# Optimization experiments

Measured on AMD Instinct MI355X. Metric: run time of the kernel, lower is better.

Reference implementation:

```python
import jax, jax.numpy as jnp
import numpy as np

B, T, DE, DD, A, FN, FS = 32, 2000, 512, 1024, 128, 32, 16
TEMPERATURE = 1.0


def setup_inputs() -> dict:
    key = jax.random.key(0)
    ks = jax.random.split(key, 10)
    input_enc = jax.random.normal(ks[0], (B, T, DE), dtype=jnp.float32)
    # lengths in [T//2, T] so no zero-length utterances
    enc_lengths = jax.random.randint(ks[1], (B,), T // 2, T + 1, dtype=jnp.int32)
    input_dec = jax.random.normal(ks[2], (B, DD), dtype=jnp.float32)
    # prev_att: previous-step attention weights (masked, normalized)
    prev_att = jax.random.uniform(ks[3], (B, T), dtype=jnp.float32)
    pad = jnp.arange(T)[None, :] >= enc_lengths[:, None]
    prev_att = jnp.where(pad, 0.0, prev_att)
    prev_att = prev_att / jnp.sum(prev_att, axis=1, keepdims=True)
    # parameters
    conv_w = jax.random.normal(ks[4], (FN, 1, 2 * FS + 1), dtype=jnp.float32) * 0.1  # [out,in,k]
    enc_w = jax.random.normal(ks[5], (A, DE), dtype=jnp.float32) * 0.04
    dec_w = jax.random.normal(ks[6], (A, DD), dtype=jnp.float32) * 0.03
    att_w = jax.random.normal(ks[7], (A, FN), dtype=jnp.float32) * 0.17
    att_b = jnp.zeros((A,), dtype=jnp.float32)
    out_w = jax.random.normal(ks[8], (1, A), dtype=jnp.float32) * 0.09
    return dict(input_enc=input_enc, enc_lengths=enc_lengths, input_dec=input_dec,
                prev_att=prev_att, conv_w=conv_w, enc_w=enc_w, dec_w=dec_w,
                att_w=att_w, att_b=att_b, out_w=out_w)


def reference(input_enc, enc_lengths, input_dec, prev_att,
              conv_w, enc_w, dec_w, att_w, att_b, out_w):
    b, t, _ = input_enc.shape
    fs = (conv_w.shape[-1] - 1) // 2  # 'same' padding
    # padding mask: True at padded positions t >= length
    mask = jnp.arange(t)[None, :] >= enc_lengths[:, None]  # [B,T]
    # location features: Conv1d over prev attention, 1 -> FN channels, same length
    conv = jax.lax.conv_general_dilated(
        prev_att[:, None, :], conv_w, window_strides=(1,),
        padding=[(fs, fs)], dimension_numbers=("NCH", "OIH", "NCH"))  # [B,FN,T]
    loc_feat = conv.transpose(0, 2, 1)  # [B,T,FN]
    projected_att = loc_feat @ att_w.T + att_b        # [B,T,A]
    projected_enc = input_enc @ enc_w.T               # [B,T,A]
    projected_dec = (input_dec @ dec_w.T)[:, None, :]  # [B,1,A]
    score = jnp.squeeze(jnp.tanh(projected_att + projected_enc + projected_dec) @ out_w.T, -1)  # [B,T]
    score = jnp.where(mask, -jnp.inf, score)
    att_weight = jax.nn.softmax(TEMPERATURE * score, axis=1)  # [B,T]
    context = jnp.einsum("btd,bt->bd", input_enc, att_weight)  # [B,DE]
    return context, att_weight
```

## Files before the change

### kernel.cpp

```cpp
#include <hip/hip_runtime.h>
#include <hip/hip_bf16.h>
#include <math.h>

#define B_ 32
#define T_ 2000
#define DE_ 512
#define DD_ 1024
#define A_ 128
#define FN_ 32
#define FS_ 16
#define KW_ (2*FS_+1)

typedef __bf16 bf16x8 __attribute__((ext_vector_type(8)));
typedef __bf16 bf16x4 __attribute__((ext_vector_type(4)));
typedef float f32x4 __attribute__((ext_vector_type(4)));

#define BT 64
#define LSTR 40

__device__ __forceinline__ void load_lds16(const void* g, void* l) {
    __builtin_amdgcn_global_load_lds(
        (const __attribute__((address_space(1))) unsigned int*)g,
        (__attribute__((address_space(3))) unsigned int*)l, 16, 0, 0);
}

__global__ __launch_bounds__(256) void prep_kernel(
    const float* __restrict__ enc_w, const float* __restrict__ att_w,
    const float* __restrict__ input_dec, const float* __restrict__ dec_w,
    const float* __restrict__ att_b,
    __bf16* __restrict__ enc_bf, __bf16* __restrict__ att_bf,
    float* __restrict__ pdec, float* __restrict__ ctx_un )
{
    int bx = blockIdx.x, tid = threadIdx.x;
    if (bx < 64) {
        int i = bx * 256 + tid;
        float4 v = ((const float4*)enc_w)[i];
        bf16x4 o;
        o[0] = (__bf16)v.x; o[1] = (__bf16)v.y; o[2] = (__bf16)v.z; o[3] = (__bf16)v.w;
        *(bf16x4*)(enc_bf + (size_t)i * 4) = o;
        if (i < (A_ * FN_) / 4) {
            float4 w = ((const float4*)att_w)[i];
            bf16x4 p;
            p[0] = (__bf16)w.x; p[1] = (__bf16)w.y; p[2] = (__bf16)w.z; p[3] = (__bf16)w.w;
            *(bf16x4*)(att_bf + (size_t)i * 4) = p;
        }
    } else if (bx < 192) {
        int pb = bx - 64;
        int b  = pb >> 2;
        int a0 = (pb & 3) * 32;
        int al = tid >> 3;
        int kg = tid & 7;
        int a  = a0 + al;
        const float4* w = (const float4*)(dec_w + (size_t)a * DD_);
        const float4* x = (const float4*)(input_dec + (size_t)b * DD_);
        float acc = 0.f;
        #pragma unroll 8
        for (int j = 0; j < 32; j++) {
            int i4 = kg + j * 8;
            float4 wv = w[i4], xv = x[i4];
            acc += wv.x * xv.x + wv.y * xv.y + wv.z * xv.z + wv.w * xv.w;
        }
        acc += __shfl_xor(acc, 1, 64);
        acc += __shfl_xor(acc, 2, 64);
        acc += __shfl_xor(acc, 4, 64);
        if (kg == 0) pdec[b * A_ + a] = acc + att_b[a];
    } else {
        int idx = (bx - 192) * 256 + tid;
        if (idx < (B_ * DE_ + B_) / 4 + 1)
            ((float4*)ctx_un)[idx] = make_float4(0.f, 0.f, 0.f, 0.f);
    }
}

__global__ __launch_bounds__(256, 4) void score_kernel(
    const float* __restrict__ input_enc, const __bf16* __restrict__ enc_bf,
    const float* __restrict__ prev_att,  const float* __restrict__ conv_w,
    const __bf16* __restrict__ att_bf,   const float* __restrict__ pdec,
    const float* __restrict__ out_w,     const int* __restrict__ lengths,
    float* __restrict__ wbuf, float* __restrict__ ctx_un,
    float* __restrict__ denom)
{
    __shared__ __align__(16) char Bt[16384];
    __shared__ float pa_s[BT + 2 * FS_];
    __shared__ float cw_s[KW_ * FN_];
    __shared__ __align__(16) __bf16 loc_s[BT * LSTR];
    __shared__ float w_s[BT];

    const int tid = threadIdx.x;
    const int b  = blockIdx.y;
    const int t0 = blockIdx.x * BT;
    const int len = lengths[b];

    for (int j = tid; j < BT + 2 * FS_; j += 256) {
        int t = t0 - FS_ + j;
        pa_s[j] = (t >= 0 && t < T_) ? prev_att[b * T_ + t] : 0.f;
    }
    for (int idx = tid; idx < FN_ * KW_; idx += 256) {
        int f = idx / KW_, k = idx % KW_;
        cw_s[k * FN_ + f] = conv_w[idx];
    }
    __syncthreads();

    {
        int f = tid & 31, r0 = tid >> 5;
        for (int r = r0; r < BT; r += 8) {
            float acc = 0.f;
            #pragma unroll
            for (int k = 0; k < KW_; k++) acc += pa_s[r + k] * cw_s[k * FN_ + f];
            loc_s[r * LSTR + f] = (__bf16)acc;
        }
    }
    __syncthreads();

    const int lane = tid & 63;
    const int wv   = tid >> 6;
    const int col  = lane & 15;
    const int grp  = lane >> 4;
    const int rowb = wv * 16 + col;
    const int t_row = t0 + rowb;
    const int t_clamp = t_row < T_ ? t_row : T_ - 1;
    const int sw = (col & 7);

    f32x4 acc[8];
    const f32x4 zero = (f32x4){0.f, 0.f, 0.f, 0.f};

    {
        bf16x8 afrag = *(const bf16x8*)(loc_s + rowb * LSTR + grp * 8);
        #pragma unroll
        for (int i = 0; i < 8; i++) {
            bf16x8 bfrag = *(const bf16x8*)(att_bf + (size_t)(i * 16 + col) * FN_ + grp * 8);
            acc[i] = __builtin_amdgcn_mfma_f32_16x16x32_bf16(afrag, bfrag, zero, 0, 0, 0);
        }
    }

    const float* arow = input_enc + ((size_t)(b * T_ + t_clamp)) * DE_ + grp * 8;

    for (int kc = 0; kc < DE_; kc += 64) {
        #pragma unroll
        for (int j = 0; j < 4; j++) {
            int s  = j * 256 + tid;
            int r  = s >> 3;
            int cp = s & 7;
            int c  = cp ^ (r & 7);
            load_lds16(enc_bf + (size_t)r * DE_ + kc + c * 8,
                       Bt + j * 4096 + wv * 1024);
        }
        float4 a00 = *(const float4*)(arow + kc);
        float4 a01 = *(const float4*)(arow + kc + 4);
        float4 a10 = *(const float4*)(arow + kc + 32);
        float4 a11 = *(const float4*)(arow + kc + 36);
        __syncthreads();

        bf16x8 af;
        af[0] = (__bf16)a00.x; af[1] = (__bf16)a00.y;
        af[2] = (__bf16)a00.z; af[3] = (__bf16)a00.w;
        af[4] = (__bf16)a01.x; af[5] = (__bf16)a01.y;
        af[6] = (__bf16)a01.z; af[7] = (__bf16)a01.w;
        #pragma unroll
        for (int i = 0; i < 8; i++) {
            bf16x8 bfrag = *(const bf16x8*)(Bt + (i * 16 + col) * 128 + ((grp ^ sw) * 16));
            acc[i] = __builtin_amdgcn_mfma_f32_16x16x32_bf16(af, bfrag, acc[i], 0, 0, 0);
        }
        af[0] = (__bf16)a10.x; af[1] = (__bf16)a10.y;
        af[2] = (__bf16)a10.z; af[3] = (__bf16)a10.w;
        af[4] = (__bf16)a11.x; af[5] = (__bf16)a11.y;
        af[6] = (__bf16)a11.z; af[7] = (__bf16)a11.w;
        #pragma unroll
        for (int i = 0; i < 8; i++) {
            bf16x8 bfrag = *(const bf16x8*)(Bt + (i * 16 + col) * 128 + (((4 + grp) ^ sw) * 16));
            acc[i] = __builtin_amdgcn_mfma_f32_16x16x32_bf16(af, bfrag, acc[i], 0, 0, 0);
        }
        __syncthreads();
    }

    float s[4] = {0.f, 0.f, 0.f, 0.f};
    float Mabs = 0.f;
    #pragma unroll
    for (int i = 0; i < 8; i++) {
        int a = i * 16 + col;
        float ow = out_w[a];
        Mabs += fabsf(ow);
        float bias = pdec[b * A_ + a];
        #pragma unroll
        for (int r = 0; r < 4; r++) {
            float v = acc[i][r] + bias;
            v = fminf(fmaxf(v, -15.f), 15.f);
            float e = __expf(2.f * v);
            s[r] += ow * ((e - 1.f) / (e + 1.f));
        }
    }
    #pragma unroll
    for (int r = 0; r < 4; r++) {
        s[r] += __shfl_xor(s[r], 1, 64);
        s[r] += __shfl_xor(s[r], 2, 64);
        s[r] += __shfl_xor(s[r], 4, 64);
        s[r] += __shfl_xor(s[r], 8, 64);
    }
    Mabs += __shfl_xor(Mabs, 1, 64);
    Mabs += __shfl_xor(Mabs, 2, 64);
    Mabs += __shfl_xor(Mabs, 4, 64);
    Mabs += __shfl_xor(Mabs, 8, 64);

    if (col == 0) {
        #pragma unroll
        for (int r = 0; r < 4; r++) {
            int rl = wv * 16 + grp * 4 + r;
            int t = t0 + rl;
            float w = 0.f;
            if (t < len) w = __expf(s[r] - Mabs);
            w_s[rl] = w;
            if (t < T_) wbuf[b * T_ + t] = w;
        }
    }
    __syncthreads();

    if (tid < 64) {
        float w = w_s[tid];
        w += __shfl_xor(w, 1, 64);
        w += __shfl_xor(w, 2, 64);
        w += __shfl_xor(w, 4, 64);
        w += __shfl_xor(w, 8, 64);
        w += __shfl_xor(w, 16, 64);
        w += __shfl_xor(w, 32, 64);
        if (tid == 0) atomicAdd(&denom[b], w);
    }

    int n_eff = len - t0;
    if (n_eff > BT) n_eff = BT;
    if (n_eff > 0) {
        int d0 = tid * 2;
        const float* ebase = input_enc + ((size_t)(b * T_ + t0)) * DE_ + d0;
        float cx = 0.f, cy = 0.f;
        #pragma unroll 8
        for (int t = 0; t < n_eff; t++) {
            float w = w_s[t];
            float2 v = *(const float2*)(ebase + (size_t)t * DE_);
            cx += w * v.x;
            cy += w * v.y;
        }
        atomicAdd(&ctx_un[b * DE_ + d0 + 0], cx);
        atomicAdd(&ctx_un[b * DE_ + d0 + 1], cy);
    }
}

__global__ __launch_bounds__(256) void finalize_kernel(
    const float* __restrict__ wbuf, const float* __restrict__ ctx_un,
    const float* __restrict__ denom, float* __restrict__ out)
{
    int bx = blockIdx.x, tid = threadIdx.x;
    if (bx < 64) {
        int i4 = bx * 256 + tid;
        if (i4 < (B_ * T_) / 4) {
            int b = i4 / (T_ / 4);
            float inv = 1.f / denom[b];
            float4 w = ((const float4*)wbuf)[i4];
            w.x *= inv; w.y *= inv; w.z *= inv; w.w *= inv;
            ((float4*)(out + B_ * DE_))[i4] = w;
        }
    } else {
        int j = (bx - 64) * 256 + tid;
        int b = j / (DE_ / 4);
        float inv = 1.f / denom[b];
        float4 c = ((const float4*)ctx_un)[j];
        c.x *= inv; c.y *= inv; c.z *= inv; c.w *= inv;
        ((float4*)out)[j] = c;
    }
}

extern "C" void kernel_launch(void* const* d_in, const int* in_sizes, int n_in,
                              void* d_out, int out_size, void* d_ws, size_t ws_size,
                              hipStream_t stream)
{
    const float* input_enc   = (const float*)d_in[0];
    const int*   enc_lengths = (const int*)d_in[1];
    const float* input_dec   = (const float*)d_in[2];
    const float* prev_att    = (const float*)d_in[3];
    const float* conv_w      = (const float*)d_in[4];
    const float* enc_w       = (const float*)d_in[5];
    const float* dec_w       = (const float*)d_in[6];
    const float* att_w       = (const float*)d_in[7];
    const float* att_b       = (const float*)d_in[8];
    const float* out_w       = (const float*)d_in[9];

    float* out = (float*)d_out;
    char* ws = (char*)d_ws;
    float*  pdec   = (float*)ws;
    float*  wbuf   = (float*)(ws + 16384);
    __bf16* enc_bf = (__bf16*)(ws + 272384);
    __bf16* att_bf = (__bf16*)(ws + 403456);
    float*  ctx_un = (float*)(ws + 411648);
    float*  denom  = (float*)(ws + 477184);

    prep_kernel<<<209, 256, 0, stream>>>(enc_w, att_w, input_dec, dec_w, att_b,
                                         enc_bf, att_bf, pdec, ctx_un);

    dim3 sgrid((T_ + BT - 1) / BT, B_);
    score_kernel<<<sgrid, 256, 0, stream>>>(input_enc, enc_bf, prev_att, conv_w,
                                            att_bf, pdec, out_w, enc_lengths,
                                            wbuf, ctx_un, denom);

    finalize_kernel<<<80, 256, 0, stream>>>(wbuf, ctx_un, denom, out);
}
```

Measured before the change: 226.6 us.

## Double-buffer encoder weight LDS tiles and register-block the location conv

Splits the shared-memory B tile into two buffers and issues the next K-chunk's async global->LDS loads and the next input_enc row loads before running the current chunk's MFMAs. This drops one barrier per iteration and overlaps memory latency with compute. The location convolution now keeps the filter taps in registers and computes 8 outputs per thread from a register window, replacing the repeated LDS reads. The cost is 16KB more LDS and higher register pressure, which may lower occupancy under launch_bounds(256,4).

```diff
diff --git a/kernel.cpp b/kernel.cpp
--- a/kernel.cpp
+++ b/kernel.cpp
@@ -79,9 +79,8 @@
     float* __restrict__ wbuf, float* __restrict__ ctx_un,
     float* __restrict__ denom)
 {
-    __shared__ __align__(16) char Bt[16384];
-    __shared__ float pa_s[BT + 2 * FS_];
-    __shared__ float cw_s[KW_ * FN_];
+    __shared__ __align__(16) char Bt[2][16384];
+    __shared__ __align__(16) float pa_s[BT + 2 * FS_];
     __shared__ __align__(16) __bf16 loc_s[BT * LSTR];
     __shared__ float w_s[BT];
 
@@ -90,24 +89,33 @@
     const int t0 = blockIdx.x * BT;
     const int len = lengths[b];
 
+    const int f    = tid & 31;
+    const int rblk = tid >> 5;
+    float cwr[KW_];
+    #pragma unroll
+    for (int k = 0; k < KW_; k++) cwr[k] = conv_w[f * KW_ + k];
+
     for (int j = tid; j < BT + 2 * FS_; j += 256) {
         int t = t0 - FS_ + j;
         pa_s[j] = (t >= 0 && t < T_) ? prev_att[b * T_ + t] : 0.f;
     }
-    for (int idx = tid; idx < FN_ * KW_; idx += 256) {
-        int f = idx / KW_, k = idx % KW_;
-        cw_s[k * FN_ + f] = conv_w[idx];
-    }
     __syncthreads();
 
     {
-        int f = tid & 31, r0 = tid >> 5;
-        for (int r = r0; r < BT; r += 8) {
-            float acc = 0.f;
+        float par[40];
+        #pragma unroll
+        for (int j = 0; j < 10; j++)
+            *(float4*)&par[j * 4] = *(const float4*)&pa_s[rblk * 8 + j * 4];
+        float accv[8] = {0.f, 0.f, 0.f, 0.f, 0.f, 0.f, 0.f, 0.f};
+        #pragma unroll
+        for (int k = 0; k < KW_; k++) {
+            float c = cwr[k];
             #pragma unroll
-            for (int k = 0; k < KW_; k++) acc += pa_s[r + k] * cw_s[k * FN_ + f];
-            loc_s[r * LSTR + f] = (__bf16)acc;
-        }
+            for (int j = 0; j < 8; j++) accv[j] += par[j + k] * c;
+        }
+        #pragma unroll
+        for (int j = 0; j < 8; j++)
+            loc_s[(rblk * 8 + j) * LSTR + f] = (__bf16)accv[j];
     }
     __syncthreads();
 
@@ -120,6 +128,16 @@
     const int t_clamp = t_row < T_ ? t_row : T_ - 1;
     const int sw = (col & 7);
 
+    #pragma unroll
+    for (int j = 0; j < 4; j++) {
+        int s  = j * 256 + tid;
+        int r  = s >> 3;
+        int cp = s & 7;
+        int c  = cp ^ (r & 7);
+        load_lds16(enc_bf + (size_t)r * DE_ + c * 8,
+                   Bt[0] + j * 4096 + wv * 1024);
+    }
+
     f32x4 acc[8];
     const f32x4 zero = (f32x4){0.f, 0.f, 0.f, 0.f};
 
@@ -134,21 +152,33 @@
 
     const float* arow = input_enc + ((size_t)(b * T_ + t_clamp)) * DE_ + grp * 8;
 
-    for (int kc = 0; kc < DE_; kc += 64) {
-        #pragma unroll
-        for (int j = 0; j < 4; j++) {
-            int s  = j * 256 + tid;
-            int r  = s >> 3;
-            int cp = s & 7;
-            int c  = cp ^ (r & 7);
-            load_lds16(enc_bf + (size_t)r * DE_ + kc + c * 8,
-                       Bt + j * 4096 + wv * 1024);
-        }
-        float4 a00 = *(const float4*)(arow + kc);
-        float4 a01 = *(const float4*)(arow + kc + 4);
-        float4 a10 = *(const float4*)(arow + kc + 32);
-        float4 a11 = *(const float4*)(arow + kc + 36);
-        __syncthreads();
+    float4 a00 = *(const float4*)(arow + 0);
+    float4 a01 = *(const float4*)(arow + 4);
+    float4 a10 = *(const float4*)(arow + 32);
+    float4 a11 = *(const float4*)(arow + 36);
+
+    __syncthreads();
+
+    int cur = 0;
+    #pragma unroll
+    for (int it = 0; it < 8; ++it) {
+        const int kc = it * 64;
+        float4 n00, n01, n10, n11;
+        if (it < 7) {
+            #pragma unroll
+            for (int j = 0; j < 4; j++) {
+                int s  = j * 256 + tid;
+                int r  = s >> 3;
+                int cp = s & 7;
+                int c  = cp ^ (r & 7);
+                load_lds16(enc_bf + (size_t)r * DE_ + (kc + 64) + c * 8,
+                           Bt[cur ^ 1] + j * 4096 + wv * 1024);
+            }
+            n00 = *(const float4*)(arow + kc + 64);
+            n01 = *(const float4*)(arow + kc + 68);
+            n10 = *(const float4*)(arow + kc + 96);
+            n11 = *(const float4*)(arow + kc + 100);
+        }
 
         bf16x8 af;
         af[0] = (__bf16)a00.x; af[1] = (__bf16)a00.y;
@@ -157,7 +187,7 @@
         af[6] = (__bf16)a01.z; af[7] = (__bf16)a01.w;
         #pragma unroll
         for (int i = 0; i < 8; i++) {
-            bf16x8 bfrag = *(const bf16x8*)(Bt + (i * 16 + col) * 128 + ((grp ^ sw) * 16));
+            bf16x8 bfrag = *(const bf16x8*)(Bt[cur] + (i * 16 + col) * 128 + ((grp ^ sw) * 16));
             acc[i] = __builtin_amdgcn_mfma_f32_16x16x32_bf16(af, bfrag, acc[i], 0, 0, 0);
         }
         af[0] = (__bf16)a10.x; af[1] = (__bf16)a10.y;
@@ -166,10 +196,13 @@
         af[6] = (__bf16)a11.z; af[7] = (__bf16)a11.w;
         #pragma unroll
         for (int i = 0; i < 8; i++) {
-            bf16x8 bfrag = *(const bf16x8*)(Bt + (i * 16 + col) * 128 + (((4 + grp) ^ sw) * 16));
+            bf16x8 bfrag = *(const bf16x8*)(Bt[cur] + (i * 16 + col) * 128 + (((4 + grp) ^ sw) * 16));
             acc[i] = __builtin_amdgcn_mfma_f32_16x16x32_bf16(af, bfrag, acc[i], 0, 0, 0);
         }
+
         __syncthreads();
+        if (it < 7) { a00 = n00; a01 = n01; a10 = n10; a11 = n11; }
+        cur ^= 1;
     }
 
     float s[4] = {0.f, 0.f, 0.f, 0.f};
```

After: 232.4 us. 1.03x slower.
